# Kernel optimization log

Measured on AMD Instinct MI355X. Metric: run time of the kernel, lower is better.

Reference implementation:

```python
import jax, jax.numpy as jnp
import numpy as np

GAMMA = 2.0
ALPHA = 0.25
SIZE_AVERAGE = True


def setup_inputs() -> dict:
    key = jax.random.key(0)
    k1, k2 = jax.random.split(key)
    B, C = 32768, 2048
    # probabilities strictly inside (0, 1) so log terms stay finite
    result = jax.random.uniform(k1, (B, C), dtype=jnp.float32,
                                minval=1e-4, maxval=1.0 - 1e-4)
    classes = jax.random.randint(k2, (B,), 0, C, dtype=jnp.int64)
    return {"result": result, "classes": classes}


def reference(result, classes):
    # nan -> 1e-6 (matches the in-place isnan patching in the original)
    p = jnp.where(jnp.isnan(result), jnp.float32(1e-6), result)  # [B, C]
    B, C = p.shape
    is_target = jax.nn.one_hot(classes, C, dtype=jnp.bool_)       # [B, C]
    # target class:     -alpha     * (1-p)^gamma * log(p)
    # non-target class: -(1-alpha) *  p^gamma    * log(1-p)
    pos = -ALPHA * jnp.power(1.0 - p, GAMMA) * jnp.log(p)
    neg = -(1.0 - ALPHA) * jnp.power(p, GAMMA) * jnp.log(1.0 - p)
    loss = jnp.sum(jnp.where(is_target, pos, neg))
    if SIZE_AVERAGE:
        loss = loss / B
    return loss
```

## Files before the change

kernel.cpp:

```cpp
#include <hip/hip_runtime.h>
#include <hip/hip_bf16.h>

static constexpr int BLOCK     = 256;
static constexpr int GRID_MAIN = 2048;
static constexpr int GRID_FIX  = 32;

__device__ __forceinline__ float patch_nan(float x) {
    return (x != x) ? 1e-6f : x;
}

__device__ __forceinline__ float neg_term(float x) {
    return -0.75f * x * x * __logf(1.0f - x);
}

__device__ __forceinline__ float pos_term(float x) {
    float om = 1.0f - x;
    return -0.25f * om * om * __logf(x);
}

__device__ __forceinline__ float block_reduce_sum(float v) {
    #pragma unroll
    for (int off = 32; off > 0; off >>= 1)
        v += __shfl_down(v, off, 64);
    __shared__ float smem[BLOCK / 64];
    const int lane = threadIdx.x & 63;
    const int wid  = threadIdx.x >> 6;
    if (lane == 0) smem[wid] = v;
    __syncthreads();
    float r = 0.0f;
    if (threadIdx.x == 0) {
        #pragma unroll
        for (int i = 0; i < BLOCK / 64; ++i) r += smem[i];
    }
    return r;
}

__global__ void __launch_bounds__(BLOCK)
focal_main(const float4* __restrict__ p4, float* __restrict__ partials, int n4) {
    float acc = 0.0f;
    const int stride = gridDim.x * blockDim.x;
    for (int i = blockIdx.x * blockDim.x + threadIdx.x; i < n4; i += stride) {
        float4 v = p4[i];
        acc += neg_term(patch_nan(v.x));
        acc += neg_term(patch_nan(v.y));
        acc += neg_term(patch_nan(v.z));
        acc += neg_term(patch_nan(v.w));
    }
    float r = block_reduce_sum(acc);
    if (threadIdx.x == 0) partials[blockIdx.x] = r;
}

__global__ void __launch_bounds__(BLOCK)
focal_fix(const float* __restrict__ p, const int* __restrict__ classes,
          float* __restrict__ partials, int B, int C) {
    float acc = 0.0f;
    const int stride = gridDim.x * blockDim.x;
    for (int b = blockIdx.x * blockDim.x + threadIdx.x; b < B; b += stride) {
        int c = classes[b];
        float x = patch_nan(p[(long long)b * C + c]);
        acc += pos_term(x) - neg_term(x);
    }
    float r = block_reduce_sum(acc);
    if (threadIdx.x == 0) partials[blockIdx.x] = r;
}

__global__ void __launch_bounds__(BLOCK)
focal_final(const float* __restrict__ partials, int n,
            float* __restrict__ out, float invB) {
    float acc = 0.0f;
    for (int i = threadIdx.x; i < n; i += blockDim.x) acc += partials[i];
    float r = block_reduce_sum(acc);
    if (threadIdx.x == 0) out[0] = r * invB;
}

extern "C" void kernel_launch(void* const* d_in, const int* in_sizes, int n_in,
                              void* d_out, int out_size, void* d_ws, size_t ws_size,
                              hipStream_t stream) {
    const float* p       = (const float*)d_in[0];
    const int*   classes = (const int*)d_in[1];
    float*       out     = (float*)d_out;
    float*       ws      = (float*)d_ws;

    const long long N = (long long)in_sizes[0];
    const int B = in_sizes[1];
    const int C = (int)(N / B);
    const int n4 = (int)(N / 4);

    float* part_main = ws;
    float* part_fix  = ws + GRID_MAIN;

    focal_main<<<GRID_MAIN, BLOCK, 0, stream>>>((const float4*)p, part_main, n4);
    focal_fix <<<GRID_FIX,  BLOCK, 0, stream>>>(p, classes, part_fix, B, C);
    focal_final<<<1, BLOCK, 0, stream>>>(ws, GRID_MAIN + GRID_FIX, out, 1.0f / (float)B);
}
```

Baseline: 55.43 us.

## Fuse target-class correction into main streaming kernel with nontemporal loads

Removes the separate gather kernel that read the target-class element for each row, and instead detects the target column inside the main streaming loop via a per-element class lookup, applying the positive-term correction in place. Loads of the probability matrix switch to nontemporal builtin loads. This drops one kernel launch and the scattered gather, but adds a classes[] read and a compare per float4, and assumes C/4 is a power of two for the shift/mask row computation.

```diff
diff --git a/kernel.cpp b/kernel.cpp
--- a/kernel.cpp
+++ b/kernel.cpp
@@ -3,7 +3,8 @@
 
 static constexpr int BLOCK     = 256;
 static constexpr int GRID_MAIN = 2048;
-static constexpr int GRID_FIX  = 32;
+
+typedef float f32x4 __attribute__((ext_vector_type(4)));
 
 __device__ __forceinline__ float patch_nan(float x) {
     return (x != x) ? 1e-6f : x;
@@ -36,29 +37,26 @@
 }
 
 __global__ void __launch_bounds__(BLOCK)
-focal_main(const float4* __restrict__ p4, float* __restrict__ partials, int n4) {
+focal_fused(const f32x4* __restrict__ p4, const int* __restrict__ classes,
+            float* __restrict__ partials, int n4, int shiftC4) {
     float acc = 0.0f;
-    const int stride = gridDim.x * blockDim.x;
+    const int maskC4  = (1 << shiftC4) - 1;
+    const int stride  = gridDim.x * blockDim.x;
     for (int i = blockIdx.x * blockDim.x + threadIdx.x; i < n4; i += stride) {
-        float4 v = p4[i];
-        acc += neg_term(patch_nan(v.x));
-        acc += neg_term(patch_nan(v.y));
-        acc += neg_term(patch_nan(v.z));
-        acc += neg_term(patch_nan(v.w));
-    }
-    float r = block_reduce_sum(acc);
-    if (threadIdx.x == 0) partials[blockIdx.x] = r;
-}
-
-__global__ void __launch_bounds__(BLOCK)
-focal_fix(const float* __restrict__ p, const int* __restrict__ classes,
-          float* __restrict__ partials, int B, int C) {
-    float acc = 0.0f;
-    const int stride = gridDim.x * blockDim.x;
-    for (int b = blockIdx.x * blockDim.x + threadIdx.x; b < B; b += stride) {
-        int c = classes[b];
-        float x = patch_nan(p[(long long)b * C + c]);
-        acc += pos_term(x) - neg_term(x);
+        f32x4 v = __builtin_nontemporal_load(&p4[i]);
+        float x0 = patch_nan(v.x), x1 = patch_nan(v.y);
+        float x2 = patch_nan(v.z), x3 = patch_nan(v.w);
+        acc += neg_term(x0);
+        acc += neg_term(x1);
+        acc += neg_term(x2);
+        acc += neg_term(x3);
+        const int row     = i >> shiftC4;
+        const int colbase = (i & maskC4) << 2;
+        const unsigned d  = (unsigned)(classes[row] - colbase);
+        if (d < 4u) {
+            float x = (d == 0) ? x0 : (d == 1) ? x1 : (d == 2) ? x2 : x3;
+            acc += pos_term(x) - neg_term(x);
+        }
     }
     float r = block_reduce_sum(acc);
     if (threadIdx.x == 0) partials[blockIdx.x] = r;
@@ -82,14 +80,15 @@
     float*       ws      = (float*)d_ws;
 
     const long long N = (long long)in_sizes[0];
-    const int B = in_sizes[1];
-    const int C = (int)(N / B);
+    const int B  = in_sizes[1];
+    const int C  = (int)(N / B);
     const int n4 = (int)(N / 4);
+    const int c4 = C / 4;
 
-    float* part_main = ws;
-    float* part_fix  = ws + GRID_MAIN;
+    int shiftC4 = 0;
+    while ((1 << shiftC4) < c4) ++shiftC4;
 
-    focal_main<<<GRID_MAIN, BLOCK, 0, stream>>>((const float4*)p, part_main, n4);
-    focal_fix <<<GRID_FIX,  BLOCK, 0, stream>>>(p, classes, part_fix, B, C);
-    focal_final<<<1, BLOCK, 0, stream>>>(ws, GRID_MAIN + GRID_FIX, out, 1.0f / (float)B);
+    focal_fused<<<GRID_MAIN, BLOCK, 0, stream>>>((const f32x4*)p, classes,
+                                                 ws, n4, shiftC4);
+    focal_final<<<1, BLOCK, 0, stream>>>(ws, GRID_MAIN, out, 1.0f / (float)B);
 }
```

After: 53.04 us. 4.3% less time.
